# Optimization experiments

Measured on AMD Instinct MI355X. Metric: run time of the kernel, lower is better.

Reference implementation:

```python
import jax, jax.numpy as jnp
import numpy as np

B, C, H, W = 8, 64, 64, 64
PROJ = 8


def setup_inputs() -> dict:
    key = jax.random.key(0)
    ks = jax.random.split(key, 8)
    inp = {
        "query_x": jax.random.normal(ks[0], (B, C, H, W), dtype=jnp.float32),
        "ref_x": jax.random.normal(ks[1], (B, C, H, W), dtype=jnp.float32),
        # 1x1 conv weights stored as [out_ch, in_ch] (kernel_size=1)
        "wq": jax.random.normal(ks[2], (PROJ, C), dtype=jnp.float32) * 0.05,
        "bq": jnp.zeros((PROJ,), dtype=jnp.float32),
        "wk": jax.random.normal(ks[3], (PROJ, C), dtype=jnp.float32) * 0.05,
        "bk": jnp.zeros((PROJ,), dtype=jnp.float32),
        "wv": jax.random.normal(ks[4], (C, C), dtype=jnp.float32) * 0.05,
        "bv": jnp.zeros((C,), dtype=jnp.float32),
    }
    return inp


def reference(query_x, ref_x, wq, bq, wk, bk, wv, bv):
    b, c, h, w = ref_x.shape
    n = h * w
    # 1x1 conv projections, flattened to [B, ch, HW]
    q = (jnp.einsum("oc,bchw->bohw", wq, query_x) + bq[None, :, None, None]).reshape(b, PROJ, n)
    k = (jnp.einsum("oc,bchw->bohw", wk, ref_x) + bk[None, :, None, None]).reshape(b, PROJ, n)
    v = (jnp.einsum("oc,bchw->bohw", wv, ref_x) + bv[None, :, None, None]).reshape(b, c, n)
    # energy[b, j(ref), i(query)] = sum_p k[b,p,j] * q[b,p,i]  (unscaled)
    energy = jnp.einsum("bpj,bpi->bji", k, q)
    attention = jax.nn.softmax(energy, axis=-1)
    # z = bmm(v, attention^T): z[b,c,j] = sum_i v[b,c,i] * attention[b,j,i]
    z = jnp.einsum("bci,bji->bcj", v, attention).reshape(b, c, h, w)
    return query_x + z
```

## Files before the change

### kernel.cpp

```cpp
#include <hip/hip_runtime.h>
#include <hip/hip_bf16.h>

#define B_ 8
#define C_ 64
#define N_ 4096
#define ITERS 32

typedef __attribute__((ext_vector_type(4))) short bf16x4;
typedef __attribute__((ext_vector_type(8))) short bf16x8;
typedef __attribute__((ext_vector_type(4))) float f32x4;

static __device__ inline ushort f2bf(float x) {
    union { float f; unsigned u; } c; c.f = x;
    return (ushort)((c.u + 0x7FFFu + ((c.u >> 16) & 1u)) >> 16);
}
static __device__ inline short f2bfs(float x) {
    __hip_bfloat16 h = __float2bfloat16(x);
    return *reinterpret_cast<short*>(&h);
}
static __device__ inline int4 pack8(const ushort* s) {
    int4 r;
    r.x = (int)(s[0] | ((unsigned)s[1] << 16));
    r.y = (int)(s[2] | ((unsigned)s[3] << 16));
    r.z = (int)(s[4] | ((unsigned)s[5] << 16));
    r.w = (int)(s[6] | ((unsigned)s[7] << 16));
    return r;
}

#if __has_builtin(__builtin_amdgcn_mfma_f32_16x16x16bf16_1k)
static __device__ inline f32x4 mfma16(bf16x4 a, bf16x4 b, f32x4 c) {
    return __builtin_amdgcn_mfma_f32_16x16x16bf16_1k(a, b, c, 0, 0, 0);
}
#else
static __device__ inline f32x4 mfma16(bf16x4 a, bf16x4 b, f32x4 c) {
    bf16x8 a8 = (bf16x8){a[0], a[1], a[2], a[3], 0, 0, 0, 0};
    bf16x8 b8 = (bf16x8){b[0], b[1], b[2], b[3], 0, 0, 0, 0};
    return __builtin_amdgcn_mfma_f32_16x16x32_bf16(a8, b8, c, 0, 0, 0);
}
#endif

__global__ __launch_bounds__(256) void proj_kernel(
    const float* __restrict__ qx, const float* __restrict__ rx,
    const float* __restrict__ wq, const float* __restrict__ bq,
    const float* __restrict__ wk, const float* __restrict__ bk,
    const float* __restrict__ wv, const float* __restrict__ bv,
    ushort* __restrict__ qb, ushort* __restrict__ kb, ushort* __restrict__ vt)
{
    const int og  = blockIdx.y;
    const int gid = blockIdx.x * 256 + threadIdx.x;
    const int b   = gid >> 12;
    const int i   = gid & (N_ - 1);

    if (og <= 1) {
        const float* xp = (og == 0 ? qx : rx) + (size_t)b * C_ * N_ + i;
        const float* wp = (og == 0 ? wq : wk);
        const float* bp = (og == 0 ? bq : bk);
        float a[8];
#pragma unroll
        for (int p = 0; p < 8; ++p) a[p] = bp[p];
        for (int c = 0; c < C_; ++c) {
            const float x = xp[(size_t)c * N_];
#pragma unroll
            for (int p = 0; p < 8; ++p) a[p] = fmaf(wp[p * C_ + c], x, a[p]);
        }
        ushort u8[8];
#pragma unroll
        for (int p = 0; p < 8; ++p) u8[p] = f2bf(a[p]);
        ushort* dst = (og == 0 ? qb : kb) + (size_t)gid * 8;
        *(int4*)dst = pack8(u8);
    } else {
        const int o0 = (og - 2) * 16;
        const float* xp = rx + (size_t)b * C_ * N_ + i;
        float a[16];
#pragma unroll
        for (int p = 0; p < 16; ++p) a[p] = bv[o0 + p];
        for (int c = 0; c < C_; ++c) {
            const float x = xp[(size_t)c * N_];
#pragma unroll
            for (int p = 0; p < 16; ++p)
                a[p] = fmaf(wv[(o0 + p) * C_ + c], x, a[p]);
        }
#pragma unroll
        for (int p = 0; p < 16; ++p)
            vt[((size_t)b * C_ + o0 + p) * N_ + i] = f2bf(a[p]);
    }
}

__global__ __launch_bounds__(512, 4) void attn_kernel(
    const ushort* __restrict__ qb, const ushort* __restrict__ kb,
    const ushort* __restrict__ vt, const float* __restrict__ qx,
    float* __restrict__ out)
{
    __shared__ __align__(16) char smem[35328];
    ushort* vbuf     = (ushort*)smem;
    float*  o_lds    = (float*)smem;
    float*  lsum_lds = (float*)(smem + 2 * 64 * 68 * 4);

    const int tid = threadIdx.x;
    const int w   = tid >> 6;
    const int ig  = w >> 1;
    const int jw  = w & 1;
    const int l   = tid & 63;
    const int cc  = l & 15;
    const int g   = l >> 4;
    const int b   = blockIdx.y;
    const int j0  = blockIdx.x * 64;

    bf16x4 bk0 = (bf16x4){0, 0, 0, 0}, bk1 = (bf16x4){0, 0, 0, 0};
    if (g < 2) {
        const ushort* kp = kb + ((size_t)b * N_ + j0 + jw * 32 + cc) * 8 + g * 4;
        bk0 = *(const bf16x4*)(kp);
        bk1 = *(const bf16x4*)(kp + 16 * 8);
    }

    const int qperm = 8 * (cc >> 2) + (cc & 3);
    const ushort* qit = qb + ((size_t)b * N_ + (size_t)ig * (N_ / 4) + qperm) * 8 + g * 4;

    const int ts  = tid & 127;
    const int sig = tid >> 7;
    const int sc  = ts >> 1;
    const int sch = ts & 1;
    const ushort* vsrc = vt + ((size_t)b * C_ + sc) * N_ + (size_t)sig * (N_ / 4) + sch * 16;
    ushort* stile = vbuf + sig * 2 * 2048;
    const int ws0 = sc * 32 + (((sch * 2 + 0) ^ (sc & 3)) << 3);
    const int ws1 = sc * 32 + (((sch * 2 + 1) ^ (sc & 3)) << 3);

    const int rbase = cc * 32 + ((g ^ (cc & 3)) << 3);

    f32x4 acc[2][4];
#pragma unroll
    for (int jb = 0; jb < 2; ++jb)
#pragma unroll
        for (int ct = 0; ct < 4; ++ct) acc[jb][ct] = (f32x4){0.f, 0.f, 0.f, 0.f};
    float lsum0 = 0.f, lsum1 = 0.f;
    const f32x4 zero4 = (f32x4){0.f, 0.f, 0.f, 0.f};

    {
        int4 a0 = *(const int4*)(vsrc);
        int4 a1 = *(const int4*)(vsrc + 8);
        *(int4*)(stile + ws0) = a0;
        *(int4*)(stile + ws1) = a1;
    }
    bf16x4 aq0 = (bf16x4){0, 0, 0, 0}, aq1 = (bf16x4){0, 0, 0, 0};
    if (g < 2) {
        aq0 = *(const bf16x4*)(qit);
        aq1 = *(const bf16x4*)(qit + 32);
    }
    __syncthreads();

    int cur = 0;
    for (int it = 0; it < ITERS; ++it) {
        const bool more = (it + 1 < ITERS);

        int4 nv0, nv1;
        if (more) {
            const ushort* s = vsrc + (size_t)(it + 1) * 32;
            nv0 = *(const int4*)(s);
            nv1 = *(const int4*)(s + 8);
        }
        bf16x4 nq0 = (bf16x4){0, 0, 0, 0}, nq1 = (bf16x4){0, 0, 0, 0};
        if (more && g < 2) {
            const ushort* s = qit + (size_t)(it + 1) * 256;
            nq0 = *(const bf16x4*)(s);
            nq1 = *(const bf16x4*)(s + 32);
        }

        f32x4 e00 = mfma16(aq0, bk0, zero4);
        f32x4 e01 = mfma16(aq1, bk0, zero4);
        f32x4 e10 = mfma16(aq0, bk1, zero4);
        f32x4 e11 = mfma16(aq1, bk1, zero4);

        float p0[8], p1[8];
#pragma unroll
        for (int r = 0; r < 4; ++r) {
            p0[r] = __expf(e00[r]); p0[4 + r] = __expf(e01[r]);
            p1[r] = __expf(e10[r]); p1[4 + r] = __expf(e11[r]);
        }
        bf16x8 pb0, pb1;
#pragma unroll
        for (int e = 0; e < 8; ++e) {
            pb0[e] = f2bfs(p0[e]);
            pb1[e] = f2bfs(p1[e]);
            lsum0 += p0[e];
            lsum1 += p1[e];
        }

        const ushort* vtile = vbuf + (ig * 2 + cur) * 2048;
#pragma unroll
        for (int ct = 0; ct < 4; ++ct) {
            bf16x8 av = *(const bf16x8*)(vtile + ct * 512 + rbase);
            acc[0][ct] = __builtin_amdgcn_mfma_f32_16x16x32_bf16(av, pb0, acc[0][ct], 0, 0, 0);
            acc[1][ct] = __builtin_amdgcn_mfma_f32_16x16x32_bf16(av, pb1, acc[1][ct], 0, 0, 0);
        }

        if (more) {
            ushort* d = stile + (cur ? 0 : 2048);
            *(int4*)(d + ws0) = nv0;
            *(int4*)(d + ws1) = nv1;
        }
        aq0 = nq0; aq1 = nq1;
        __syncthreads();
        cur ^= 1;
    }

    lsum0 += __shfl_xor(lsum0, 16, 64);
    lsum0 += __shfl_xor(lsum0, 32, 64);
    lsum1 += __shfl_xor(lsum1, 16, 64);
    lsum1 += __shfl_xor(lsum1, 32, 64);

    const int jl = jw * 32 + cc;
    if (ig < 2) {
        float* od = o_lds + ig * (64 * 68);
#pragma unroll
        for (int ct = 0; ct < 4; ++ct)
#pragma unroll
            for (int r = 0; r < 4; ++r) {
                od[(ct * 16 + 4 * g + r) * 68 + jl]      = acc[0][ct][r];
                od[(ct * 16 + 4 * g + r) * 68 + jl + 16] = acc[1][ct][r];
            }
        if (g == 0) {
            lsum_lds[ig * 64 + jl]      = lsum0;
            lsum_lds[ig * 64 + jl + 16] = lsum1;
        }
    }
    __syncthreads();
    if (ig >= 2) {
        float* od = o_lds + (ig - 2) * (64 * 68);
#pragma unroll
        for (int ct = 0; ct < 4; ++ct)
#pragma unroll
            for (int r = 0; r < 4; ++r) {
                od[(ct * 16 + 4 * g + r) * 68 + jl]      += acc[0][ct][r];
                od[(ct * 16 + 4 * g + r) * 68 + jl + 16] += acc[1][ct][r];
            }
        if (g == 0) {
            lsum_lds[(ig - 2) * 64 + jl]      += lsum0;
            lsum_lds[(ig - 2) * 64 + jl + 16] += lsum1;
        }
    }
    __syncthreads();

    const int ec = tid >> 3;
    const int ej = (tid & 7) * 8;
    const float* xp = qx  + ((size_t)b * C_ + ec) * N_ + j0 + ej;
    float*       op = out + ((size_t)b * C_ + ec) * N_ + j0 + ej;
    float4 x0 = *(const float4*)xp;
    float4 x1 = *(const float4*)(xp + 4);
    float rr[8];
#pragma unroll
    for (int t = 0; t < 8; ++t) {
        const float num = o_lds[ec * 68 + ej + t] + o_lds[64 * 68 + ec * 68 + ej + t];
        const float den = lsum_lds[ej + t] + lsum_lds[64 + ej + t];
        rr[t] = num / den;
    }
    float4 r0 = make_float4(x0.x + rr[0], x0.y + rr[1], x0.z + rr[2], x0.w + rr[3]);
    float4 r1 = make_float4(x1.x + rr[4], x1.y + rr[5], x1.z + rr[6], x1.w + rr[7]);
    *(float4*)op       = r0;
    *(float4*)(op + 4) = r1;
}

extern "C" void kernel_launch(void* const* d_in, const int* in_sizes, int n_in,
                              void* d_out, int out_size, void* d_ws, size_t ws_size,
                              hipStream_t stream) {
    const float* qx = (const float*)d_in[0];
    const float* rx = (const float*)d_in[1];
    const float* wq = (const float*)d_in[2];
    const float* bq = (const float*)d_in[3];
    const float* wk = (const float*)d_in[4];
    const float* bk = (const float*)d_in[5];
    const float* wv = (const float*)d_in[6];
    const float* bv = (const float*)d_in[7];
    float* out = (float*)d_out;

    ushort* qb = (ushort*)d_ws;
    ushort* kb = qb + (size_t)B_ * N_ * 8;
    ushort* vt = kb + (size_t)B_ * N_ * 8;

    proj_kernel<<<dim3((B_ * N_) / 256, 6), 256, 0, stream>>>(
        qx, rx, wq, bq, wk, bk, wv, bv, qb, kb, vt);

    attn_kernel<<<dim3(N_ / 64, B_), 512, 0, stream>>>(qb, kb, vt, qx, out);
}
```

Measured before the change: 60.43 us.

## Load V straight into registers, drop LDS staging and barriers, use exp2

The attention loop now loads the V operand for its MFMAs directly from global memory into registers, with one-iteration-ahead prefetch. This replaces the double-buffered LDS tile and the per-iteration __syncthreads. The K projection is pre-scaled by log2(e) so the softmax exponent can use the hardware exp2 builtin. The V projection now computes 32 output channels per thread over 2 grid rows instead of 16 over 4. In exchange, the two waves that share an i-group each fetch the same V data from cache, Q is loaded for all lanes (the extra lanes are multiplied by zero K), and the projection kernel uses more registers per thread.

```diff
diff --git a/kernel.cpp b/kernel.cpp
--- a/kernel.cpp
+++ b/kernel.cpp
@@ -25,6 +25,14 @@
     r.z = (int)(s[4] | ((unsigned)s[5] << 16));
     r.w = (int)(s[6] | ((unsigned)s[7] << 16));
     return r;
+}
+
+static __device__ inline float exp2fast(float x) {
+#if __has_builtin(__builtin_amdgcn_exp2f)
+    return __builtin_amdgcn_exp2f(x);
+#else
+    return exp2f(x);
+#endif
 }
 
 #if __has_builtin(__builtin_amdgcn_mfma_f32_16x16x16bf16_1k)
@@ -55,6 +63,7 @@
         const float* xp = (og == 0 ? qx : rx) + (size_t)b * C_ * N_ + i;
         const float* wp = (og == 0 ? wq : wk);
         const float* bp = (og == 0 ? bq : bk);
+        const float scale = (og == 0) ? 1.0f : 1.44269504088896340736f;
         float a[8];
 #pragma unroll
         for (int p = 0; p < 8; ++p) a[p] = bp[p];
@@ -65,23 +74,23 @@
         }
         ushort u8[8];
 #pragma unroll
-        for (int p = 0; p < 8; ++p) u8[p] = f2bf(a[p]);
+        for (int p = 0; p < 8; ++p) u8[p] = f2bf(a[p] * scale);
         ushort* dst = (og == 0 ? qb : kb) + (size_t)gid * 8;
         *(int4*)dst = pack8(u8);
     } else {
-        const int o0 = (og - 2) * 16;
+        const int o0 = (og - 2) * 32;
         const float* xp = rx + (size_t)b * C_ * N_ + i;
-        float a[16];
-#pragma unroll
-        for (int p = 0; p < 16; ++p) a[p] = bv[o0 + p];
+        float a[32];
+#pragma unroll
+        for (int p = 0; p < 32; ++p) a[p] = bv[o0 + p];
         for (int c = 0; c < C_; ++c) {
             const float x = xp[(size_t)c * N_];
 #pragma unroll
-            for (int p = 0; p < 16; ++p)
+            for (int p = 0; p < 32; ++p)
                 a[p] = fmaf(wv[(o0 + p) * C_ + c], x, a[p]);
         }
 #pragma unroll
-        for (int p = 0; p < 16; ++p)
+        for (int p = 0; p < 32; ++p)
             vt[((size_t)b * C_ + o0 + p) * N_ + i] = f2bf(a[p]);
     }
 }
@@ -91,10 +100,8 @@
     const ushort* __restrict__ vt, const float* __restrict__ qx,
     float* __restrict__ out)
 {
-    __shared__ __align__(16) char smem[35328];
-    ushort* vbuf     = (ushort*)smem;
-    float*  o_lds    = (float*)smem;
-    float*  lsum_lds = (float*)(smem + 2 * 64 * 68 * 4);
+    __shared__ float o_lds[2 * 64 * 68];
+    __shared__ float lsum_lds[2 * 64];
 
     const int tid = threadIdx.x;
     const int w   = tid >> 6;
@@ -114,18 +121,8 @@
     }
 
     const int qperm = 8 * (cc >> 2) + (cc & 3);
-    const ushort* qit = qb + ((size_t)b * N_ + (size_t)ig * (N_ / 4) + qperm) * 8 + g * 4;
-
-    const int ts  = tid & 127;
-    const int sig = tid >> 7;
-    const int sc  = ts >> 1;
-    const int sch = ts & 1;
-    const ushort* vsrc = vt + ((size_t)b * C_ + sc) * N_ + (size_t)sig * (N_ / 4) + sch * 16;
-    ushort* stile = vbuf + sig * 2 * 2048;
-    const int ws0 = sc * 32 + (((sch * 2 + 0) ^ (sc & 3)) << 3);
-    const int ws1 = sc * 32 + (((sch * 2 + 1) ^ (sc & 3)) << 3);
-
-    const int rbase = cc * 32 + ((g ^ (cc & 3)) << 3);
+    const ushort* qptr = qb + ((size_t)b * N_ + (size_t)ig * (N_ / 4) + qperm) * 8 + g * 4;
+    const ushort* vptr = vt + ((size_t)b * C_ + cc) * N_ + (size_t)ig * (N_ / 4) + g * 8;
 
     f32x4 acc[2][4];
 #pragma unroll
@@ -135,35 +132,24 @@
     float lsum0 = 0.f, lsum1 = 0.f;
     const f32x4 zero4 = (f32x4){0.f, 0.f, 0.f, 0.f};
 
-    {
-        int4 a0 = *(const int4*)(vsrc);
-        int4 a1 = *(const int4*)(vsrc + 8);
-        *(int4*)(stile + ws0) = a0;
-        *(int4*)(stile + ws1) = a1;
-    }
-    bf16x4 aq0 = (bf16x4){0, 0, 0, 0}, aq1 = (bf16x4){0, 0, 0, 0};
-    if (g < 2) {
-        aq0 = *(const bf16x4*)(qit);
-        aq1 = *(const bf16x4*)(qit + 32);
-    }
-    __syncthreads();
-
-    int cur = 0;
+    bf16x8 v0 = *(const bf16x8*)(vptr);
+    bf16x8 v1 = *(const bf16x8*)(vptr + 16 * N_);
+    bf16x8 v2 = *(const bf16x8*)(vptr + 32 * N_);
+    bf16x8 v3 = *(const bf16x8*)(vptr + 48 * N_);
+    bf16x4 aq0 = *(const bf16x4*)(qptr);
+    bf16x4 aq1 = *(const bf16x4*)(qptr + 32);
+
+#pragma unroll 2
     for (int it = 0; it < ITERS; ++it) {
-        const bool more = (it + 1 < ITERS);
-
-        int4 nv0, nv1;
-        if (more) {
-            const ushort* s = vsrc + (size_t)(it + 1) * 32;
-            nv0 = *(const int4*)(s);
-            nv1 = *(const int4*)(s + 8);
-        }
-        bf16x4 nq0 = (bf16x4){0, 0, 0, 0}, nq1 = (bf16x4){0, 0, 0, 0};
-        if (more && g < 2) {
-            const ushort* s = qit + (size_t)(it + 1) * 256;
-            nq0 = *(const bf16x4*)(s);
-            nq1 = *(const bf16x4*)(s + 32);
-        }
+        const int nxt = (it + 1) & (ITERS - 1);
+        const ushort* vp = vptr + nxt * 32;
+        bf16x8 nv0 = *(const bf16x8*)(vp);
+        bf16x8 nv1 = *(const bf16x8*)(vp + 16 * N_);
+        bf16x8 nv2 = *(const bf16x8*)(vp + 32 * N_);
+        bf16x8 nv3 = *(const bf16x8*)(vp + 48 * N_);
+        const ushort* qp = qptr + nxt * 256;
+        bf16x4 nq0 = *(const bf16x4*)(qp);
+        bf16x4 nq1 = *(const bf16x4*)(qp + 32);
 
         f32x4 e00 = mfma16(aq0, bk0, zero4);
         f32x4 e01 = mfma16(aq1, bk0, zero4);
@@ -173,8 +159,8 @@
         float p0[8], p1[8];
 #pragma unroll
         for (int r = 0; r < 4; ++r) {
-            p0[r] = __expf(e00[r]); p0[4 + r] = __expf(e01[r]);
-            p1[r] = __expf(e10[r]); p1[4 + r] = __expf(e11[r]);
+            p0[r] = exp2fast(e00[r]); p0[4 + r] = exp2fast(e01[r]);
+            p1[r] = exp2fast(e10[r]); p1[4 + r] = exp2fast(e11[r]);
         }
         bf16x8 pb0, pb1;
 #pragma unroll
@@ -185,22 +171,17 @@
             lsum1 += p1[e];
         }
 
-        const ushort* vtile = vbuf + (ig * 2 + cur) * 2048;
-#pragma unroll
-        for (int ct = 0; ct < 4; ++ct) {
-            bf16x8 av = *(const bf16x8*)(vtile + ct * 512 + rbase);
-            acc[0][ct] = __builtin_amdgcn_mfma_f32_16x16x32_bf16(av, pb0, acc[0][ct], 0, 0, 0);
-            acc[1][ct] = __builtin_amdgcn_mfma_f32_16x16x32_bf16(av, pb1, acc[1][ct], 0, 0, 0);
-        }
-
-        if (more) {
-            ushort* d = stile + (cur ? 0 : 2048);
-            *(int4*)(d + ws0) = nv0;
-            *(int4*)(d + ws1) = nv1;
-        }
+        acc[0][0] = __builtin_amdgcn_mfma_f32_16x16x32_bf16(v0, pb0, acc[0][0], 0, 0, 0);
+        acc[1][0] = __builtin_amdgcn_mfma_f32_16x16x32_bf16(v0, pb1, acc[1][0], 0, 0, 0);
+        acc[0][1] = __builtin_amdgcn_mfma_f32_16x16x32_bf16(v1, pb0, acc[0][1], 0, 0, 0);
+        acc[1][1] = __builtin_amdgcn_mfma_f32_16x16x32_bf16(v1, pb1, acc[1][1], 0, 0, 0);
+        acc[0][2] = __builtin_amdgcn_mfma_f32_16x16x32_bf16(v2, pb0, acc[0][2], 0, 0, 0);
+        acc[1][2] = __builtin_amdgcn_mfma_f32_16x16x32_bf16(v2, pb1, acc[1][2], 0, 0, 0);
+        acc[0][3] = __builtin_amdgcn_mfma_f32_16x16x32_bf16(v3, pb0, acc[0][3], 0, 0, 0);
+        acc[1][3] = __builtin_amdgcn_mfma_f32_16x16x32_bf16(v3, pb1, acc[1][3], 0, 0, 0);
+
+        v0 = nv0; v1 = nv1; v2 = nv2; v3 = nv3;
         aq0 = nq0; aq1 = nq1;
-        __syncthreads();
-        cur ^= 1;
     }
 
     lsum0 += __shfl_xor(lsum0, 16, 64);
@@ -276,7 +257,7 @@
     ushort* kb = qb + (size_t)B_ * N_ * 8;
     ushort* vt = kb + (size_t)B_ * N_ * 8;
 
-    proj_kernel<<<dim3((B_ * N_) / 256, 6), 256, 0, stream>>>(
+    proj_kernel<<<dim3((B_ * N_) / 256, 4), 256, 0, stream>>>(
         qx, rx, wq, bq, wk, bk, wv, bv, qb, kb, vt);
 
     attn_kernel<<<dim3(N_ / 64, B_), 512, 0, stream>>>(qb, kb, vt, qx, out);
```

Measured after the change: 91.41 us. 1.51x slower.
